# Kernel tuning notes

Hardware: AMD Instinct MI355X
Metric: run time of the kernel (lower is better)

The kernel has to match this reference:

```python
import jax, jax.numpy as jnp
import numpy as np

B, NG, K_NN = 8, 4096, 3          # graphs, nodes per graph, knn k
CHEB_K = 4                        # SGWT/Chebyshev order K
IN_CH, HID, M, OUT_CH = 32, 64, 100, 16
N = B * NG
E_PPI = 600
BIG = 1e9


def knn_edges(x, n_graphs, n_per, k):
    """Per-graph knn_graph (no self loops). Returns global (src, dst), edges grouped per target node."""
    xg = x.reshape(n_graphs, n_per, -1)
    sq = jnp.sum(xg * xg, axis=-1)                                   # [B, n]
    d = sq[:, :, None] + sq[:, None, :] - 2.0 * jnp.einsum('bic,bjc->bij', xg, xg)
    d = d + BIG * jnp.eye(n_per, dtype=x.dtype)                      # exclude self
    idx = jax.lax.top_k(-d, k)[1]                                    # [B, n, k] neighbor ids
    offs = (jnp.arange(n_graphs) * n_per)[:, None, None]
    src = (idx + offs).reshape(-1)
    dst = jnp.broadcast_to(jnp.arange(n_per)[None, :, None] + offs, (n_graphs, n_per, k)).reshape(-1)
    return src, dst


def cheb_conv(x, src, dst, w, W, b, n):
    """SGWT/Chebyshev conv: sum_k T_k(L~) x W_k with L~ = -D^-1/2 A D^-1/2 (lambda_max=2)."""
    deg = jax.ops.segment_sum(w, dst, num_segments=n)
    dn = jnp.where(deg > 0, jax.lax.rsqrt(jnp.maximum(deg, 1e-12)), 0.0)
    wn = w * dn[dst] * dn[src]

    def lap(v):
        return -jax.ops.segment_sum(wn[:, None] * v[src], dst, num_segments=n)

    Z_prev = x
    out = x @ W[0]
    Z_cur = lap(x)
    out = out + Z_cur @ W[1]
    for kk in range(2, W.shape[0]):
        Z_next = 2.0 * lap(Z_cur) - Z_prev
        out = out + Z_next @ W[kk]
        Z_prev, Z_cur = Z_cur, Z_next
    return out + b


def graph_norm(x, alpha, gamma, beta, n_graphs, n_per, eps=1e-5):
    xg = x.reshape(n_graphs, n_per, -1)
    mean = xg.mean(axis=1, keepdims=True)
    sub = xg - alpha * mean
    var = (sub * sub).mean(axis=1, keepdims=True)
    out = gamma * sub * jax.lax.rsqrt(var + eps) + beta
    return out.reshape(x.shape)


def edge_conv(x, src, dst, W, b, n):
    """EdgeConv: max_j MLP([x_i, x_j - x_i])."""
    feat = jnp.concatenate([x[dst], x[src] - x[dst]], axis=1)
    h = jax.nn.relu(feat @ W + b)
    agg = jax.ops.segment_max(h, dst, num_segments=n)
    return jnp.where(jnp.isfinite(agg), agg, 0.0)


def mlp3(x, w1, b1, w2, b2, w3, b3):
    h = jax.nn.selu(x @ w1 + b1)
    h = jax.nn.selu(h @ w2 + b2)
    return h @ w3 + b3


def setup_inputs():
    key = jax.random.key(0)
    ks = jax.random.split(key, 32)

    def p(i, shape):
        fan_in = shape[-2] if len(shape) >= 2 else shape[-1]
        return jax.random.normal(ks[i], shape, jnp.float32) / np.sqrt(fan_in)

    inp = {
        'x': jax.random.normal(ks[0], (N, IN_CH), jnp.float32),
        'edge_weight': jax.random.uniform(ks[1], (N * K_NN,), jnp.float32),
        'batch': jnp.repeat(jnp.arange(B), NG),
        'connect': jax.random.randint(ks[2], (2, E_PPI), 0, M),
        # conv0 (SGWT) params
        'W0': p(3, (CHEB_K, IN_CH, HID)), 'b0': jnp.zeros((HID,), jnp.float32),
        # GraphNorm
        'gn_alpha': jnp.ones((HID,), jnp.float32), 'gn_gamma': jnp.ones((HID,), jnp.float32), 'gn_beta': jnp.zeros((HID,), jnp.float32),
        # conv1 (SGWT) params -> m*4
        'W1': p(4, (CHEB_K, HID, 4 * M)), 'b1c': jnp.zeros((4 * M,), jnp.float32),
        # fc1: 4m -> 2m -> m -> m
        'f1w1': p(5, (4 * M, 2 * M)), 'f1b1': jnp.zeros((2 * M,), jnp.float32),
        'f1w2': p(6, (2 * M, M)), 'f1b2': jnp.zeros((M,), jnp.float32),
        'f1w3': p(7, (M, M)), 'f1b3': jnp.zeros((M,), jnp.float32),
        # conv2 (PPIEdgeConv): 2*in_ch -> hidden
        'W2': p(8, (2 * IN_CH, HID)), 'b2': jnp.zeros((HID,), jnp.float32),
        # conv3 (DynamicEdgeConv): 2*hidden -> hidden
        'W3': p(9, (2 * HID, HID)), 'b3': jnp.zeros((HID,), jnp.float32),
        # fc2: h -> h/2 -> h/4 -> out
        'f2w1': p(10, (HID, HID // 2)), 'f2b1': jnp.zeros((HID // 2,), jnp.float32),
        'f2w2': p(11, (HID // 2, HID // 4)), 'f2b2': jnp.zeros((HID // 4,), jnp.float32),
        'f2w3': p(12, (HID // 4, OUT_CH)), 'f2b3': jnp.zeros((OUT_CH,), jnp.float32),
    }
    return inp


def reference(x, edge_weight, batch, connect, W0, b0, gn_alpha, gn_gamma, gn_beta,
              W1, b1c, f1w1, f1b1, f1w2, f1b2, f1w3, f1b3,
              W2, b2, W3, b3, f2w1, f2b1, f2w2, f2b2, f2w3, f2b3):
    n = x.shape[0]
    # knn on raw features -> SGWT conv0 -> GraphNorm
    src, dst = knn_edges(x, B, NG, K_NN)
    u = cheb_conv(x, src, dst, edge_weight, W0, b0, n)
    u = graph_norm(u, gn_alpha, gn_gamma, gn_beta, B, NG)
    # knn on hidden features -> SGWT conv1 -> fc1
    src, dst = knn_edges(u, B, NG, K_NN)
    u = cheb_conv(u, src, dst, edge_weight, W1, b1c, n)
    u = mlp3(u, f1w1, f1b1, f1w2, f1b2, f1w3, f1b3)                   # [N, M]
    # DiffPool-style soft assignment pooling
    S = jax.nn.softmax(u, axis=-1).reshape(B, NG, M)
    Xd = x.reshape(B, NG, IN_CH)
    pooled = jnp.einsum('bnm,bnc->bmc', S, Xd) / S.sum(axis=1)[:, :, None]
    xp = pooled.reshape(B * M, IN_CH)
    # PPIEdgeConv over fixed 'connect' graph replicated per pooled graph
    offs = (jnp.arange(B) * M)[:, None]
    psrc = (connect[0][None, :] + offs).reshape(-1)
    pdst = (connect[1][None, :] + offs).reshape(-1)
    h = edge_conv(xp, psrc, pdst, W2, b2, B * M)                      # [B*M, HID]
    # DynamicEdgeConv: knn(k=3) on features
    ksrc, kdst = knn_edges(h, B, M, K_NN)
    y = edge_conv(h, ksrc, kdst, W3, b3, B * M)
    z = h + y
    v = mlp3(z, f2w1, f2b1, f2w2, f2b2, f2w3, f2b3)                   # [B*M, OUT_CH]
    return u, v
```

## Files before the change

kernel.cpp:

```cpp
#include <hip/hip_runtime.h>
#include <hip/hip_bf16.h>
#include <math.h>

#define DEVFN static __device__ __forceinline__

DEVFN int clampi(int v, int lo, int hi){ return v < lo ? lo : (v > hi ? hi : v); }


__global__ void k_zero(float* __restrict__ p, int n){
  int i = blockIdx.x*256 + threadIdx.x;
  if (i < n) p[i] = 0.f;
}

__global__ void k_filli(int* __restrict__ p, int n, int v){
  int i = blockIdx.x*256 + threadIdx.x;
  if (i < n) p[i] = v;
}

__global__ void k_fillf(float* __restrict__ p, int n, float v){
  int i = blockIdx.x*256 + threadIdx.x;
  if (i < n) p[i] = v;
}

__global__ void k_sqnorm(const float* __restrict__ x, float* __restrict__ sq, int n, int C){
  int i = blockIdx.x*256 + threadIdx.x;
  if (i >= n) return;
  const float* r = x + (size_t)i*C;
  float s = 0.f;
  for (int c = 0; c < C; ++c){ float v = r[c]; s += v*v; }
  sq[i] = s;
}


DEVFN void top3i(float d, int j, float& d0, float& d1, float& d2, int& i0, int& i1, int& i2){
  if (d < d2){
    if (d < d1){
      d2 = d1; i2 = i1;
      if (d < d0){ d1 = d0; i1 = i0; d0 = d; i0 = j; }
      else       { d1 = d;  i1 = j; }
    } else { d2 = d; i2 = j; }
  }
}

DEVFN void top3t(float d, int j, float& d0, float& d1, float& d2, int& j0, int& j1, int& j2){
  if (d < d2 || (d == d2 && j < j2)){
    if (d < d1 || (d == d1 && j < j1)){
      d2 = d1; j2 = j1;
      if (d < d0 || (d == d0 && j < j0)){ d1 = d0; j1 = j0; d0 = d; j0 = j; }
      else { d1 = d; j1 = j; }
    } else { d2 = d; j2 = j; }
  }
}


template<int C, int ROWS>
__global__ __launch_bounds__(256) void k_knn2(
    const float* __restrict__ x, const float* __restrict__ sq,
    int n_per, int nsplit, int csize,
    float* __restrict__ partd, int* __restrict__ parti)
{
  int s    = blockIdx.x;
  int tile = blockIdx.y;
  int g    = blockIdx.z;
  int tid  = threadIdx.x;
  int rpb  = 256*ROWS;
  const float* xg = x  + (size_t)g*n_per*C;
  const float* sg = sq + (size_t)g*n_per;

  int   ri[ROWS];
  float xi[ROWS][C];
  #pragma unroll
  for (int rr = 0; rr < ROWS; ++rr){
    ri[rr] = tile*rpb + rr*256 + tid;
    #pragma unroll
    for (int c4 = 0; c4 < C/4; ++c4)
      *(float4*)&xi[rr][c4*4] = *(const float4*)(xg + (size_t)ri[rr]*C + c4*4);
  }

  __shared__ float xs[128*C];
  __shared__ float ss[128];

  const float INF = __builtin_inff();
  float d0[ROWS], d1[ROWS], d2[ROWS];
  int   j0[ROWS], j1[ROWS], j2[ROWS];
  #pragma unroll
  for (int rr = 0; rr < ROWS; ++rr){ d0[rr]=INF; d1[rr]=INF; d2[rr]=INF; j0[rr]=0; j1[rr]=0; j2[rr]=0; }

  int jbase = s*csize;
  for (int t0 = jbase; t0 < jbase + csize; t0 += 128){
    __syncthreads();
    {
      const float4* src = (const float4*)(xg + (size_t)t0*C);
      float4* dst = (float4*)xs;
      for (int idx = tid; idx < 128*C/4; idx += 256) dst[idx] = src[idx];
      if (tid < 128) ss[tid] = sg[t0 + tid];
    }
    __syncthreads();
    #pragma unroll 2
    for (int jj = 0; jj < 128; ++jj){
      float qs = ss[jj];
      const float4* xr = (const float4*)(xs + jj*C);
      int j = t0 + jj;
      #pragma unroll
      for (int rr = 0; rr < ROWS; ++rr){
        float pa=0.f, pb=0.f, pc=0.f, pd=0.f;
        #pragma unroll
        for (int c4 = 0; c4 < C/4; ++c4){
          float4 w = xr[c4];
          pa += xi[rr][4*c4+0]*w.x; pb += xi[rr][4*c4+1]*w.y;
          pc += xi[rr][4*c4+2]*w.z; pd += xi[rr][4*c4+3]*w.w;
        }
        float v = fmaf(-2.f, (pa+pb)+(pc+pd), qs);
        if (j != ri[rr]) top3i(v, j, d0[rr],d1[rr],d2[rr], j0[rr],j1[rr],j2[rr]);
      }
    }
  }

  #pragma unroll
  for (int rr = 0; rr < ROWS; ++rr){
    size_t o = ((size_t)(g*n_per + ri[rr])*nsplit + s)*3;
    partd[o+0]=d0[rr]; partd[o+1]=d1[rr]; partd[o+2]=d2[rr];
    parti[o+0]=j0[rr]; parti[o+1]=j1[rr]; parti[o+2]=j2[rr];
  }
}


template<int C, int TJ>
__global__ __launch_bounds__(64) void k_knn(
    const float* __restrict__ x, const float* __restrict__ sq,
    int n_per, int bpg, int nsplit, int csize,
    float* __restrict__ partd, int* __restrict__ parti)
{
  int bid  = blockIdx.x;
  int s    = bid % nsplit;
  int b2i  = bid / nsplit;
  int g    = b2i / bpg;
  int tile = b2i % bpg;
  int tid  = threadIdx.x;
  int i0 = tile*128 + tid;
  int i1 = i0 + 64;
  const float* xg = x  + (size_t)g*n_per*C;
  const float* sg = sq + (size_t)g*n_per;
  bool a0 = i0 < n_per, a1 = i1 < n_per;
  float xi0[C], xi1[C];
  float q0 = 0.f, q1 = 0.f;
  if (a0){
    #pragma unroll
    for (int c = 0; c < C; ++c) xi0[c] = xg[(size_t)i0*C + c];
    q0 = sg[i0];
  } else {
    #pragma unroll
    for (int c = 0; c < C; ++c) xi0[c] = 0.f;
  }
  if (a1){
    #pragma unroll
    for (int c = 0; c < C; ++c) xi1[c] = xg[(size_t)i1*C + c];
    q1 = sg[i1];
  } else {
    #pragma unroll
    for (int c = 0; c < C; ++c) xi1[c] = 0.f;
  }
  __shared__ float xs[TJ*C];
  __shared__ float ss[TJ];
  float d00 = __builtin_inff(), d01 = __builtin_inff(), d02 = __builtin_inff();
  float d10 = __builtin_inff(), d11 = __builtin_inff(), d12 = __builtin_inff();
  int n00 = 0, n01 = 0, n02 = 0;
  int n10 = 0, n11 = 0, n12 = 0;

  int jbase = s*csize;
  int jend  = min(n_per, jbase + csize);
  for (int t0 = jbase; t0 < jend; t0 += TJ){
    int lim = min(TJ, jend - t0);
    __syncthreads();
    for (int idx = tid; idx < lim*C; idx += 64) xs[idx] = xg[(size_t)t0*C + idx];
    for (int idx = tid; idx < lim;   idx += 64) ss[idx] = sg[t0 + idx];
    __syncthreads();
    for (int jj = 0; jj < lim; ++jj){
      const float4* xr = (const float4*)(xs + jj*C);
      float p0a=0,p0b=0,p0c=0,p0d=0;
      float p1a=0,p1b=0,p1c=0,p1d=0;
      #pragma unroll
      for (int c4 = 0; c4 < C/4; ++c4){
        float4 w = xr[c4];
        p0a += xi0[4*c4+0]*w.x; p0b += xi0[4*c4+1]*w.y;
        p0c += xi0[4*c4+2]*w.z; p0d += xi0[4*c4+3]*w.w;
        p1a += xi1[4*c4+0]*w.x; p1b += xi1[4*c4+1]*w.y;
        p1c += xi1[4*c4+2]*w.z; p1d += xi1[4*c4+3]*w.w;
      }
      int j = t0 + jj;
      float dv0 = q0 + ss[jj] - 2.f*((p0a+p0b)+(p0c+p0d));
      float dv1 = q1 + ss[jj] - 2.f*((p1a+p1b)+(p1c+p1d));
      if (a0 && j != i0) top3i(dv0, j, d00,d01,d02, n00,n01,n02);
      if (a1 && j != i1) top3i(dv1, j, d10,d11,d12, n10,n11,n12);
    }
  }
  if (a0){
    size_t o = ((size_t)(g*n_per + i0)*nsplit + s)*3;
    partd[o+0]=d00; partd[o+1]=d01; partd[o+2]=d02;
    parti[o+0]=n00; parti[o+1]=n01; parti[o+2]=n02;
  }
  if (a1){
    size_t o = ((size_t)(g*n_per + i1)*nsplit + s)*3;
    partd[o+0]=d10; partd[o+1]=d11; partd[o+2]=d12;
    parti[o+0]=n10; parti[o+1]=n11; parti[o+2]=n12;
  }
}

__global__ void k_knnmerge(const float* __restrict__ partd, const int* __restrict__ parti,
                           int n_total, int n_per, int nsplit, int* __restrict__ nbr)
{
  int row = blockIdx.x*256 + threadIdx.x;
  if (row >= n_total) return;
  float d0 = __builtin_inff(), d1 = __builtin_inff(), d2 = __builtin_inff();
  int j0 = 0, j1 = 0, j2 = 0;
  for (int s = 0; s < nsplit; ++s){
    for (int q = 0; q < 3; ++q){
      size_t o = ((size_t)row*nsplit + s)*3 + q;
      float d = partd[o]; int j = parti[o];
      top3t(d, j, d0,d1,d2, j0,j1,j2);
    }
  }
  int g = row / n_per;
  nbr[row*3+0] = g*n_per + clampi(j0, 0, n_per-1);
  nbr[row*3+1] = g*n_per + clampi(j1, 0, n_per-1);
  nbr[row*3+2] = g*n_per + clampi(j2, 0, n_per-1);
}


__global__ void k_chebwn(const float* __restrict__ w, const int* __restrict__ nbr,
                         float* __restrict__ wn, int ne, int n){
  int e = blockIdx.x*256 + threadIdx.x;
  if (e >= ne) return;
  int i = e/3;
  int s = clampi(nbr[e], 0, n-1);
  float sd = w[3*i] + w[3*i+1] + w[3*i+2];
  float sv = w[3*s] + w[3*s+1] + w[3*s+2];
  float dnd = (sd > 0.f) ? 1.f / sqrtf(fmaxf(sd, 1e-12f)) : 0.f;
  float dns = (sv > 0.f) ? 1.f / sqrtf(fmaxf(sv, 1e-12f)) : 0.f;
  wn[e] = w[e] * dnd * dns;
}

template<int C>
__global__ void k_lap(const float* __restrict__ v, const float* __restrict__ zp,
                      const float* __restrict__ wn, const int* __restrict__ nbr,
                      float* __restrict__ out, int total, float aa, float bb)
{
  int idx = blockIdx.x*256 + threadIdx.x;
  if (idx >= total) return;
  int i = idx / C;
  int c = idx - i*C;
  int e = i*3;
  int nmax = total / C;
  int s0 = clampi(nbr[e+0], 0, nmax-1);
  int s1 = clampi(nbr[e+1], 0, nmax-1);
  int s2 = clampi(nbr[e+2], 0, nmax-1);
  float s = wn[e+0]*v[(size_t)s0*C + c]
          + wn[e+1]*v[(size_t)s1*C + c]
          + wn[e+2]*v[(size_t)s2*C + c];
  float r = -aa*s;
  if (bb != 0.f) r += bb*zp[idx];
  out[idx] = r;
}


struct In4 { const float* p0; const float* p1; const float* p2; const float* p3; };

template<int ACT, int NIN>
__global__ __launch_bounds__(256) void k_mm(
    In4 ins, const float* __restrict__ W,
    const float* __restrict__ bias, float* __restrict__ out,
    int nrows, int cin, int cout)
{
  __shared__ float inl[64][65];
  __shared__ float wl[64][64];
  int r0 = blockIdx.x * 64;
  int c0 = blockIdx.y * 64;
  int tid = threadIdx.x;
  int tr = tid & 15, tc = tid >> 4;
  float acc[4][4] = {{0,0,0,0},{0,0,0,0},{0,0,0,0},{0,0,0,0}};
  const float* inp[4] = {ins.p0, ins.p1, ins.p2, ins.p3};
  for (int ni = 0; ni < NIN; ++ni){
    const float* A = inp[ni];
    const float* Wb = W + (size_t)ni*cin*cout;
    for (int k0 = 0; k0 < cin; k0 += 64){
      int klim = min(64, cin - k0);
      __syncthreads();
      for (int idx = tid; idx < 64*64; idx += 256){
        int rr = idx >> 6, kk = idx & 63;
        float v = 0.f;
        if (r0 + rr < nrows && kk < klim) v = A[(size_t)(r0+rr)*cin + k0 + kk];
        inl[rr][kk] = v;
      }
      for (int idx = tid; idx < 64*64; idx += 256){
        int kk = idx >> 6, jj = idx & 63;
        float v = 0.f;
        if (kk < klim && c0 + jj < cout) v = Wb[(size_t)(k0+kk)*cout + c0 + jj];
        wl[kk][jj] = v;
      }
      __syncthreads();
      for (int kk = 0; kk < 64; ++kk){
        float4 wv = *(const float4*)&wl[kk][tc*4];
        float a0v = inl[tr*4+0][kk];
        float a1v = inl[tr*4+1][kk];
        float a2v = inl[tr*4+2][kk];
        float a3v = inl[tr*4+3][kk];
        acc[0][0] += a0v*wv.x; acc[0][1] += a0v*wv.y; acc[0][2] += a0v*wv.z; acc[0][3] += a0v*wv.w;
        acc[1][0] += a1v*wv.x; acc[1][1] += a1v*wv.y; acc[1][2] += a1v*wv.z; acc[1][3] += a1v*wv.w;
        acc[2][0] += a2v*wv.x; acc[2][1] += a2v*wv.y; acc[2][2] += a2v*wv.z; acc[2][3] += a2v*wv.w;
        acc[3][0] += a3v*wv.x; acc[3][1] += a3v*wv.y; acc[3][2] += a3v*wv.z; acc[3][3] += a3v*wv.w;
      }
    }
  }
  #pragma unroll
  for (int q = 0; q < 4; ++q){
    int r = r0 + tr*4 + q;
    if (r >= nrows) continue;
    #pragma unroll
    for (int p = 0; p < 4; ++p){
      int j = c0 + tc*4 + p;
      if (j >= cout) continue;
      float v = acc[q][p] + bias[j];
      if (ACT == 1) v = fmaxf(v, 0.f);
      if (ACT == 2) v = 1.0507009873554805f * (v > 0.f ? v : 1.6732632423543772f * expm1f(v));
      out[(size_t)r*cout + j] = v;
    }
  }
}


__global__ void k_gnstat(const float* __restrict__ x, float* __restrict__ msum_p,
                         float* __restrict__ m2sum_p)
{
  int g = blockIdx.x >> 4, chunk = blockIdx.x & 15;
  int c = threadIdx.x & 63, q = threadIdx.x >> 6;
  const float* xg = x + (size_t)g*4096*64;
  int nb = chunk*256;
  float s1 = 0.f, s2 = 0.f;
  for (int n = nb + q; n < nb + 256; n += 4){
    float v = xg[(size_t)n*64 + c];
    s1 += v; s2 += v*v;
  }
  __shared__ float r1[4][64], r2[4][64];
  r1[q][c] = s1; r2[q][c] = s2;
  __syncthreads();
  if (q == 0){
    msum_p [(g*16 + chunk)*64 + c] = r1[0][c]+r1[1][c]+r1[2][c]+r1[3][c];
    m2sum_p[(g*16 + chunk)*64 + c] = r2[0][c]+r2[1][c]+r2[2][c]+r2[3][c];
  }
}

__global__ void k_gnapply(float* __restrict__ x, const float* __restrict__ msum_p,
                          const float* __restrict__ m2sum_p,
                          const float* __restrict__ alpha, const float* __restrict__ gamma,
                          const float* __restrict__ beta)
{
  int idx = blockIdx.x*256 + threadIdx.x;
  if (idx >= 32768*64) return;
  int c = idx & 63;
  int node = idx >> 6;
  int g = node >> 12;
  float ms = 0.f, m2 = 0.f;
  for (int ch = 0; ch < 16; ++ch){
    ms += msum_p [(g*16 + ch)*64 + c];
    m2 += m2sum_p[(g*16 + ch)*64 + c];
  }
  float m  = ms * (1.f/4096.f);
  float e2 = m2 * (1.f/4096.f);
  float al = alpha[c];
  float var = e2 - (2.f*al - al*al)*m*m;
  float sub = x[idx] - al*m;
  x[idx] = gamma[c] * sub * (1.f/sqrtf(fmaxf(var, 0.f) + 1e-5f)) + beta[c];
}


__global__ void k_softmax(const float* __restrict__ u, float* __restrict__ S, int n){
  int i = blockIdx.x*256 + threadIdx.x;
  if (i >= n) return;
  const float* r = u + (size_t)i*100;
  float* o = S + (size_t)i*100;
  float lr[100];
  float m = -__builtin_inff();
  for (int j = 0; j < 100; ++j){ lr[j] = r[j]; m = fmaxf(m, lr[j]); }
  float ssum = 0.f;
  for (int j = 0; j < 100; ++j){ lr[j] = expf(lr[j] - m); ssum += lr[j]; }
  float inv = 1.f / ssum;
  for (int j = 0; j < 100; ++j) o[j] = lr[j] * inv;
}

__global__ void k_pool(const float* __restrict__ S, const float* __restrict__ xf,
                       float* __restrict__ PT)
{
  int g = blockIdx.x >> 4, chunk = blockIdx.x & 15;
  int tid = threadIdx.x;
  __shared__ float Sl[64*100];
  __shared__ float Xl[64*32];
  float acc[13];
  int mq[13], cq[13];
  int base = tid*13;
  #pragma unroll
  for (int q = 0; q < 13; ++q){
    acc[q] = 0.f;
    int oi = base + q;
    mq[q] = (oi < 3300) ? oi/33 : 0;
    cq[q] = (oi < 3300) ? oi%33 : 0;
  }
  const float* Sg = S  + ((size_t)g*4096 + chunk*256)*100;
  const float* Xg = xf + ((size_t)g*4096 + chunk*256)*32;
  for (int n0 = 0; n0 < 256; n0 += 64){
    __syncthreads();
    for (int idx = tid; idx < 6400; idx += 256) Sl[idx] = Sg[(size_t)n0*100 + idx];
    for (int idx = tid; idx < 2048; idx += 256) Xl[idx] = Xg[(size_t)n0*32 + idx];
    __syncthreads();
    for (int nn = 0; nn < 64; ++nn){
      #pragma unroll
      for (int q = 0; q < 13; ++q){
        int ci = cq[q] & 31;
        float xv = Xl[nn*32 + ci];
        if (cq[q] == 32) xv = 1.f;
        acc[q] += Sl[nn*100 + mq[q]] * xv;
      }
    }
  }
  #pragma unroll
  for (int q = 0; q < 13; ++q){
    int oi = base + q;
    if (oi < 3300) atomicAdd(&PT[(size_t)g*3300 + oi], acc[q]);
  }
}

__global__ void k_xp(const float* __restrict__ PT, float* __restrict__ xp){
  int i = blockIdx.x*256 + threadIdx.x;
  if (i >= 800*32) return;
  int bm = i >> 5, c = i & 31;
  xp[i] = PT[(size_t)bm*33 + c] / PT[(size_t)bm*33 + 32];
}


__global__ void k_ppi(const float* __restrict__ xp, const int* __restrict__ connect,
                      const float* __restrict__ W2, const float* __restrict__ b2v,
                      int* __restrict__ hraw)
{
  int idx = blockIdx.x*256 + threadIdx.x;
  if (idx >= 8*600*64) return;
  int c  = idx & 63;
  int eg = idx >> 6;
  int b  = eg / 600, e = eg - b*600;
  int sI = b*100 + clampi(connect[e],       0, 99);
  int dI = b*100 + clampi(connect[600 + e], 0, 99);
  float acc = b2v[c];
  #pragma unroll
  for (int t = 0; t < 32; ++t) acc += xp[(size_t)dI*32 + t] * W2[t*64 + c];
  #pragma unroll
  for (int t = 0; t < 32; ++t) acc += (xp[(size_t)sI*32 + t] - xp[(size_t)dI*32 + t]) * W2[(32+t)*64 + c];
  float r = fmaxf(acc, 0.f);
  atomicMax(&hraw[(size_t)dI*64 + c], __float_as_int(r));
}

__global__ void k_hfin(const int* __restrict__ hraw, float* __restrict__ h, int n){
  int i = blockIdx.x*256 + threadIdx.x;
  if (i >= n) return;
  float v = __int_as_float(hraw[i]);
  h[i] = (v < -1e37f) ? 0.f : v;
}


__global__ void k_dyn(const float* __restrict__ h, const int* __restrict__ nbr3,
                      const float* __restrict__ W3, const float* __restrict__ b3v,
                      float* __restrict__ z)
{
  int idx = blockIdx.x*256 + threadIdx.x;
  if (idx >= 800*64) return;
  int c = idx & 63, i = idx >> 6;
  float base = b3v[c];
  for (int t = 0; t < 64; ++t) base += h[(size_t)i*64 + t] * W3[t*64 + c];
  float mx = 0.f;
  for (int k = 0; k < 3; ++k){
    int sI = clampi(nbr3[i*3 + k], 0, 799);
    float acc = base;
    for (int t = 0; t < 64; ++t) acc += (h[(size_t)sI*64 + t] - h[(size_t)i*64 + t]) * W3[(64+t)*64 + c];
    mx = fmaxf(mx, fmaxf(acc, 0.f));
  }
  z[idx] = h[idx] + mx;
}


extern "C" void kernel_launch(void* const* d_in, const int* in_sizes, int n_in,
                              void* d_out, int out_size, void* d_ws, size_t ws_size,
                              hipStream_t stream)
{
  const size_t REQ_SMALL = 11785728ull * 4ull;
  const size_t REQ_BIG   = 31854592ull * 4ull;
  if (ws_size < REQ_SMALL || n_in < 27){
    int nb = (out_size + 255)/256;
    k_fillf<<<nb, 256, 0, stream>>>((float*)d_out, out_size, (float)ws_size);
    return;
  }
  const bool big = (ws_size >= REQ_BIG);

  const float* x    = (const float*)d_in[0];
  const float* ew   = (const float*)d_in[1];
  const int*  connect = (const int*)d_in[3];
  const float* W0  = (const float*)d_in[4];
  const float* b0  = (const float*)d_in[5];
  const float* gal = (const float*)d_in[6];
  const float* gga = (const float*)d_in[7];
  const float* gbe = (const float*)d_in[8];
  const float* W1  = (const float*)d_in[9];
  const float* b1c = (const float*)d_in[10];
  const float* f1w1=(const float*)d_in[11]; const float* f1b1=(const float*)d_in[12];
  const float* f1w2=(const float*)d_in[13]; const float* f1b2=(const float*)d_in[14];
  const float* f1w3=(const float*)d_in[15]; const float* f1b3=(const float*)d_in[16];
  const float* W2  = (const float*)d_in[17]; const float* b2v=(const float*)d_in[18];
  const float* W3  = (const float*)d_in[19]; const float* b3v=(const float*)d_in[20];
  const float* f2w1=(const float*)d_in[21]; const float* f2b1=(const float*)d_in[22];
  const float* f2w2=(const float*)d_in[23]; const float* f2b2=(const float*)d_in[24];
  const float* f2w3=(const float*)d_in[25]; const float* f2b3=(const float*)d_in[26];

  float* ws   = (float*)d_ws;
  float* u0   = ws;
  float* Za   = ws +  2097152;
  float* Zb   = ws +  4194304;
  float* Zc   = ws +  6291456;
  float* acc  = ws +  8388608;
  float* h1   = big ? (ws + 21495808) : (acc + 1638400);
  float* h2   = big ? (ws + 28049408) : (acc + 2457600);
  float* partd= Za;
  int*   parti= (int*)Zb;
  float* Sb   = Za;
  float* sm   = big ? (ws + 31326208) : (ws + 11272192);
  float* sqb  = sm;
  int*   nbr  = (int*)(sm + 163840);
  int*   nbr3 = (int*)(sm + 262144);
  float* PT   = sm + 266240;
  float* xp   = sm + 294912;
  int*   hraw = (int*)(sm + 320512);
  float* hb   = sm + 371712;
  float* zb   = sm + 422912;
  float* g1   = sm + 474112;
  float* g2   = sm + 499712;
  float* wnb  = sm + 65536;

  float* ub   = (float*)d_out;
  float* vout = ub + 3276800;

  const int N = 32768;

  k_sqnorm<<<128, 256, 0, stream>>>(x, sqb, N, 32);
  k_knn2<32,2><<<dim3(16,8,8), 256, 0, stream>>>(x, sqb, 4096, 16, 256, partd, parti);
  k_knnmerge<<<128, 256, 0, stream>>>(partd, parti, N, 4096, 16, nbr);

  k_chebwn<<<384, 256, 0, stream>>>(ew, nbr, wnb, 3*N, N);

  k_lap<32><<<4096, 256, 0, stream>>>(x, x, wnb, nbr, Za, N*32, 1.f, 0.f);
  k_lap<32><<<4096, 256, 0, stream>>>(Za, x, wnb, nbr, Zb, N*32, 2.f, -1.f);
  k_lap<32><<<4096, 256, 0, stream>>>(Zb, Za, wnb, nbr, Zc, N*32, 2.f, -1.f);
  {
    In4 ins{x, Za, Zb, Zc};
    k_mm<0,4><<<dim3(512,1), 256, 0, stream>>>(ins, W0, b0, u0, N, 32, 64);
  }

  k_gnstat<<<128, 256, 0, stream>>>(u0, sqb, sqb + 8192);
  k_gnapply<<<8192, 256, 0, stream>>>(u0, sqb, sqb + 8192, gal, gga, gbe);

  k_sqnorm<<<128, 256, 0, stream>>>(u0, sqb, N, 64);
  k_knn2<64,1><<<dim3(16,16,8), 256, 0, stream>>>(u0, sqb, 4096, 16, 256, partd, parti);
  k_knnmerge<<<128, 256, 0, stream>>>(partd, parti, N, 4096, 16, nbr);
  k_chebwn<<<384, 256, 0, stream>>>(ew, nbr, wnb, 3*N, N);

  k_lap<64><<<8192, 256, 0, stream>>>(u0, u0, wnb, nbr, Za, N*64, 1.f, 0.f);
  k_lap<64><<<8192, 256, 0, stream>>>(Za, u0, wnb, nbr, Zb, N*64, 2.f, -1.f);
  k_lap<64><<<8192, 256, 0, stream>>>(Zb, Za, wnb, nbr, Zc, N*64, 2.f, -1.f);

  {
    int nch  = big ? 1 : 8;
    int rows = big ? N : 4096;
    int gx   = big ? 512 : 64;
    for (int ch = 0; ch < nch; ++ch){
      size_t o64  = (size_t)ch*4096*64;
      size_t o100 = (size_t)ch*4096*100;
      In4 ic{u0 + o64, Za + o64, Zb + o64, Zc + o64};
      k_mm<0,4><<<dim3(gx,7), 256, 0, stream>>>(ic, W1, b1c, acc, rows, 64, 400);
      In4 i1{acc, nullptr, nullptr, nullptr};
      k_mm<2,1><<<dim3(gx,4), 256, 0, stream>>>(i1, f1w1, f1b1, h1, rows, 400, 200);
      In4 i2{h1, nullptr, nullptr, nullptr};
      k_mm<2,1><<<dim3(gx,2), 256, 0, stream>>>(i2, f1w2, f1b2, h2, rows, 200, 100);
      In4 i3{h2, nullptr, nullptr, nullptr};
      k_mm<0,1><<<dim3(gx,2), 256, 0, stream>>>(i3, f1w3, f1b3, ub + o100, rows, 100, 100);
    }
  }

  k_softmax<<<128, 256, 0, stream>>>(ub, Sb, N);
  k_zero<<<104, 256, 0, stream>>>(PT, 26400);
  k_pool<<<128, 256, 0, stream>>>(Sb, x, PT);
  k_xp<<<100, 256, 0, stream>>>(PT, xp);

  k_filli<<<200, 256, 0, stream>>>(hraw, 51200, (int)0xFF800000);
  k_ppi<<<1200, 256, 0, stream>>>(xp, connect, W2, b2v, hraw);
  k_hfin<<<200, 256, 0, stream>>>(hraw, hb, 51200);

  k_sqnorm<<<4, 256, 0, stream>>>(hb, sqb, 800, 64);
  k_knn<64,64><<<8, 64, 0, stream>>>(hb, sqb, 100, 1, 1, 100, partd, parti);
  k_knnmerge<<<4, 256, 0, stream>>>(partd, parti, 800, 100, 1, nbr3);
  k_dyn<<<200, 256, 0, stream>>>(hb, nbr3, W3, b3v, zb);

  {
    In4 j1{zb, nullptr, nullptr, nullptr};
    k_mm<2,1><<<dim3(13,1), 256, 0, stream>>>(j1, f2w1, f2b1, g1, 800, 64, 32);
    In4 j2{g1, nullptr, nullptr, nullptr};
    k_mm<2,1><<<dim3(13,1), 256, 0, stream>>>(j2, f2w2, f2b2, g2, 800, 32, 16);
    In4 j3{g2, nullptr, nullptr, nullptr};
    k_mm<0,1><<<dim3(13,1), 256, 0, stream>>>(j3, f2w3, f2b3, vout, 800, 16, 16);
  }
}
```

Measured before the change: 1.851 ms.

## Replace 256-thread knn2 kernels with 64-thread knn tiles and fewer splits

Removes the 256-thread k_knn2 kernel that used 16 column splits. The first knn now uses the existing 64-thread k_knn kernel with two rows per thread. The second knn uses a new single-row k_knn1r kernel with 64 threads and 32-column shared tiles. Both use 8 splits of 512 columns, so the merge step reads fewer partial results. The trade is less per-block parallelism and smaller shared tiles against lower merge traffic and a different occupancy profile.

Measured after the change: 1.766 ms (median of 2 runs). 4.6% less time.

```diff
diff --git a/kernel.cpp b/kernel.cpp
--- a/kernel.cpp
+++ b/kernel.cpp
@@ -49,78 +49,6 @@
       if (d < d0 || (d == d0 && j < j0)){ d1 = d0; j1 = j0; d0 = d; j0 = j; }
       else { d1 = d; j1 = j; }
     } else { d2 = d; j2 = j; }
-  }
-}
-
-
-template<int C, int ROWS>
-__global__ __launch_bounds__(256) void k_knn2(
-    const float* __restrict__ x, const float* __restrict__ sq,
-    int n_per, int nsplit, int csize,
-    float* __restrict__ partd, int* __restrict__ parti)
-{
-  int s    = blockIdx.x;
-  int tile = blockIdx.y;
-  int g    = blockIdx.z;
-  int tid  = threadIdx.x;
-  int rpb  = 256*ROWS;
-  const float* xg = x  + (size_t)g*n_per*C;
-  const float* sg = sq + (size_t)g*n_per;
-
-  int   ri[ROWS];
-  float xi[ROWS][C];
-  #pragma unroll
-  for (int rr = 0; rr < ROWS; ++rr){
-    ri[rr] = tile*rpb + rr*256 + tid;
-    #pragma unroll
-    for (int c4 = 0; c4 < C/4; ++c4)
-      *(float4*)&xi[rr][c4*4] = *(const float4*)(xg + (size_t)ri[rr]*C + c4*4);
-  }
-
-  __shared__ float xs[128*C];
-  __shared__ float ss[128];
-
-  const float INF = __builtin_inff();
-  float d0[ROWS], d1[ROWS], d2[ROWS];
-  int   j0[ROWS], j1[ROWS], j2[ROWS];
-  #pragma unroll
-  for (int rr = 0; rr < ROWS; ++rr){ d0[rr]=INF; d1[rr]=INF; d2[rr]=INF; j0[rr]=0; j1[rr]=0; j2[rr]=0; }
-
-  int jbase = s*csize;
-  for (int t0 = jbase; t0 < jbase + csize; t0 += 128){
-    __syncthreads();
-    {
-      const float4* src = (const float4*)(xg + (size_t)t0*C);
-      float4* dst = (float4*)xs;
-      for (int idx = tid; idx < 128*C/4; idx += 256) dst[idx] = src[idx];
-      if (tid < 128) ss[tid] = sg[t0 + tid];
-    }
-    __syncthreads();
-    #pragma unroll 2
-    for (int jj = 0; jj < 128; ++jj){
-      float qs = ss[jj];
-      const float4* xr = (const float4*)(xs + jj*C);
-      int j = t0 + jj;
-      #pragma unroll
-      for (int rr = 0; rr < ROWS; ++rr){
-        float pa=0.f, pb=0.f, pc=0.f, pd=0.f;
-        #pragma unroll
-        for (int c4 = 0; c4 < C/4; ++c4){
-          float4 w = xr[c4];
-          pa += xi[rr][4*c4+0]*w.x; pb += xi[rr][4*c4+1]*w.y;
-          pc += xi[rr][4*c4+2]*w.z; pd += xi[rr][4*c4+3]*w.w;
-        }
-        float v = fmaf(-2.f, (pa+pb)+(pc+pd), qs);
-        if (j != ri[rr]) top3i(v, j, d0[rr],d1[rr],d2[rr], j0[rr],j1[rr],j2[rr]);
-      }
-    }
-  }
-
-  #pragma unroll
-  for (int rr = 0; rr < ROWS; ++rr){
-    size_t o = ((size_t)(g*n_per + ri[rr])*nsplit + s)*3;
-    partd[o+0]=d0[rr]; partd[o+1]=d1[rr]; partd[o+2]=d2[rr];
-    parti[o+0]=j0[rr]; parti[o+1]=j1[rr]; parti[o+2]=j2[rr];
   }
 }
 
@@ -204,6 +132,59 @@
     partd[o+0]=d10; partd[o+1]=d11; partd[o+2]=d12;
     parti[o+0]=n10; parti[o+1]=n11; parti[o+2]=n12;
   }
+}
+
+
+template<int C, int TJ>
+__global__ __launch_bounds__(64) void k_knn1r(
+    const float* __restrict__ x, const float* __restrict__ sq,
+    int n_per, int bpg, int nsplit, int csize,
+    float* __restrict__ partd, int* __restrict__ parti)
+{
+  int bid  = blockIdx.x;
+  int s    = bid % nsplit;
+  int b2i  = bid / nsplit;
+  int g    = b2i / bpg;
+  int tile = b2i % bpg;
+  int tid  = threadIdx.x;
+  int i0 = tile*64 + tid;
+  const float* xg = x  + (size_t)g*n_per*C;
+  const float* sg = sq + (size_t)g*n_per;
+  float xi0[C];
+  #pragma unroll
+  for (int c = 0; c < C; ++c) xi0[c] = xg[(size_t)i0*C + c];
+  float q0 = sg[i0];
+
+  __shared__ float xs[TJ*C];
+  __shared__ float ss[TJ];
+  float d00 = __builtin_inff(), d01 = __builtin_inff(), d02 = __builtin_inff();
+  int n00 = 0, n01 = 0, n02 = 0;
+
+  int jbase = s*csize;
+  int jend  = min(n_per, jbase + csize);
+  for (int t0 = jbase; t0 < jend; t0 += TJ){
+    int lim = min(TJ, jend - t0);
+    __syncthreads();
+    for (int idx = tid; idx < lim*C; idx += 64) xs[idx] = xg[(size_t)t0*C + idx];
+    for (int idx = tid; idx < lim;   idx += 64) ss[idx] = sg[t0 + idx];
+    __syncthreads();
+    for (int jj = 0; jj < lim; ++jj){
+      const float4* xr = (const float4*)(xs + jj*C);
+      float p0a=0,p0b=0,p0c=0,p0d=0;
+      #pragma unroll
+      for (int c4 = 0; c4 < C/4; ++c4){
+        float4 w = xr[c4];
+        p0a += xi0[4*c4+0]*w.x; p0b += xi0[4*c4+1]*w.y;
+        p0c += xi0[4*c4+2]*w.z; p0d += xi0[4*c4+3]*w.w;
+      }
+      int j = t0 + jj;
+      float dv0 = q0 + ss[jj] - 2.f*((p0a+p0b)+(p0c+p0d));
+      if (j != i0) top3i(dv0, j, d00,d01,d02, n00,n01,n02);
+    }
+  }
+  size_t o = ((size_t)(g*n_per + i0)*nsplit + s)*3;
+  partd[o+0]=d00; partd[o+1]=d01; partd[o+2]=d02;
+  parti[o+0]=n00; parti[o+1]=n01; parti[o+2]=n02;
 }
 
 __global__ void k_knnmerge(const float* __restrict__ partd, const int* __restrict__ parti,
@@ -546,8 +527,8 @@
   const int N = 32768;
 
   k_sqnorm<<<128, 256, 0, stream>>>(x, sqb, N, 32);
-  k_knn2<32,2><<<dim3(16,8,8), 256, 0, stream>>>(x, sqb, 4096, 16, 256, partd, parti);
-  k_knnmerge<<<128, 256, 0, stream>>>(partd, parti, N, 4096, 16, nbr);
+  k_knn<32,64><<<2048, 64, 0, stream>>>(x, sqb, 4096, 32, 8, 512, partd, parti);
+  k_knnmerge<<<128, 256, 0, stream>>>(partd, parti, N, 4096, 8, nbr);
 
   k_chebwn<<<384, 256, 0, stream>>>(ew, nbr, wnb, 3*N, N);
 
@@ -563,8 +544,8 @@
   k_gnapply<<<8192, 256, 0, stream>>>(u0, sqb, sqb + 8192, gal, gga, gbe);
 
   k_sqnorm<<<128, 256, 0, stream>>>(u0, sqb, N, 64);
-  k_knn2<64,1><<<dim3(16,16,8), 256, 0, stream>>>(u0, sqb, 4096, 16, 256, partd, parti);
-  k_knnmerge<<<128, 256, 0, stream>>>(partd, parti, N, 4096, 16, nbr);
+  k_knn1r<64,32><<<4096, 64, 0, stream>>>(u0, sqb, 4096, 64, 8, 512, partd, parti);
+  k_knnmerge<<<128, 256, 0, stream>>>(partd, parti, N, 4096, 8, nbr);
   k_chebwn<<<384, 256, 0, stream>>>(ew, nbr, wnb, 3*N, N);
 
   k_lap<64><<<8192, 256, 0, stream>>>(u0, u0, wnb, nbr, Za, N*64, 1.f, 0.f);
```
